# Kernel optimization log

Measured on AMD Instinct MI355X. Metric: run time of the kernel, lower is better.

Reference implementation:

```python
import jax, jax.numpy as jnp
import numpy as np

N = 100000
E = 1600000
NEG_SLOPE = 0.2


def _gat_layer(x, src, dst, W, a_src, a_dst, b, heads, out_ch):
    n = x.shape[0]
    h = (x @ W).reshape(n, heads, out_ch)                      # [N,H,C]
    alpha_src = (h * a_src).sum(-1)                            # [N,H]
    alpha_dst = (h * a_dst).sum(-1)                            # [N,H]
    e = jax.nn.leaky_relu(alpha_src[src] + alpha_dst[dst], NEG_SLOPE)  # [E,H]
    # segment softmax over incoming edges of each destination node
    m = jax.ops.segment_max(e, dst, num_segments=n)            # [N,H]
    ex = jnp.exp(e - m[dst])
    denom = jax.ops.segment_sum(ex, dst, num_segments=n)       # [N,H]
    alpha = ex / (denom[dst] + 1e-16)                          # [E,H]
    msg = h[src] * alpha[:, :, None]                           # [E,H,C]
    out = jax.ops.segment_sum(msg, dst, num_segments=n)        # [N,H,C]
    return out.reshape(n, heads * out_ch) + b


def setup_inputs() -> dict:
    key = jax.random.key(0)
    ks = jax.random.split(key, 10)
    glorot = lambda k, shape: jax.random.normal(k, shape, jnp.float32) * np.sqrt(2.0 / (shape[0] + shape[-1]))
    x = jax.random.normal(ks[0], (N, 5), jnp.float32)
    edge_index = jax.random.randint(ks[1], (2, E), 0, N, jnp.int64)
    return {
        "x": x,
        "edge_index": edge_index,
        "W1": glorot(ks[2], (5, 64)),
        "a_src1": glorot(ks[3], (8, 8)),
        "a_dst1": glorot(ks[4], (8, 8)),
        "b1": jnp.zeros((64,), jnp.float32),
        "W2": glorot(ks[5], (64, 2)),
        "a_src2": glorot(ks[6], (1, 2)),
        "a_dst2": glorot(ks[7], (1, 2)),
        "b2": jnp.zeros((2,), jnp.float32),
    }


def reference(x, edge_index, W1, a_src1, a_dst1, b1, W2, a_src2, a_dst2, b2):
    n = x.shape[0]
    loop = jnp.arange(n, dtype=edge_index.dtype)
    src = jnp.concatenate([edge_index[0], loop])   # PyG GATConv adds self-loops
    dst = jnp.concatenate([edge_index[1], loop])
    # dropout layers are no-ops in eval mode
    h = jax.nn.elu(_gat_layer(x, src, dst, W1, a_src1, a_dst1, b1, heads=8, out_ch=8))
    out = _gat_layer(h, src, dst, W2, a_src2, a_dst2, b2, heads=1, out_ch=2)
    return jax.nn.log_softmax(out, axis=1)
```

## Files before the change

### kernel.cpp

```cpp
#include <hip/hip_runtime.h>
#include <hip/hip_fp16.h>
#include <math.h>
#include <stdint.h>

#define N_NODES 100000
#define N_EDGES 1600000
#define NEG_SLOPE 0.2f
#define LOG2E 1.44269504088896340736f

#define CB     128
#define CBBITS 7
#define NCB    ((N_NODES + CB - 1) / CB)
#define TP     2048
#define NPB    ((N_EDGES + TP - 1) / TP)
#define WINB   2560
#define NB_NODE1 ((N_NODES * 8 + 511) / 512)
#define N8     ((size_t)N_NODES * 8)

typedef int nt_int4 __attribute__((ext_vector_type(4)));

__global__ void __launch_bounds__(512) k_np(
        const int* __restrict__ src, const int* __restrict__ dst,
        int* __restrict__ ofsT, unsigned* __restrict__ pairs,
        const float* __restrict__ x, const float* __restrict__ W1,
        const float* __restrict__ a_src1, const float* __restrict__ a_dst1,
        __half* __restrict__ xh, __half* __restrict__ as1h,
        float* __restrict__ ad1) {
    __shared__ int lcnt[1024];
    __shared__ unsigned stage[TP];
    __shared__ int wred[8];
    int t = threadIdx.x;

    if (blockIdx.x >= NPB) {
        int gid  = (blockIdx.x - NPB) * 512 + t;
        int n    = gid >> 3;
        int head = gid & 7;
        if (n >= N_NODES) return;

        float xv[5];
#pragma unroll
        for (int k = 0; k < 5; ++k) xv[k] = x[n * 5 + k];

        float as = 0.f, ad = 0.f;
#pragma unroll
        for (int j = 0; j < 8; ++j) {
            int c = head * 8 + j;
            float acc = 0.f;
#pragma unroll
            for (int k = 0; k < 5; ++k) acc += xv[k] * W1[k * 64 + c];
            as += acc * a_src1[c];
            ad += acc * a_dst1[c];
        }
        as1h[n * 8 + head] = __float2half(as * LOG2E);
        ad1[n * 8 + head] = ad * LOG2E;

        if (head == 0) {
            __half2 p0 = __halves2half2(__float2half(xv[0]), __float2half(xv[1]));
            __half2 p1 = __halves2half2(__float2half(xv[2]), __float2half(xv[3]));
            __half2 p2 = __halves2half2(__float2half(xv[4]), __float2half(0.f));
            __half2 p3 = __halves2half2(__float2half(0.f), __float2half(0.f));
            __half2* xp = (__half2*)&xh[(size_t)n * 8];
            xp[0] = p0; xp[1] = p1; xp[2] = p2; xp[3] = p3;
        }
        return;
    }

    int blk = blockIdx.x;
    int base = blk * TP + t * 4;
    bool act = base < N_EDGES;
    int nE = min(TP, N_EDGES - blk * TP);

    lcnt[t] = 0; lcnt[t + 512] = 0;
    __syncthreads();

    nt_int4 s4, d4;
    int myidx[4];
    if (act) {
        s4 = __builtin_nontemporal_load((const nt_int4*)(src + base));
        d4 = __builtin_nontemporal_load((const nt_int4*)(dst + base));
#pragma unroll
        for (int j = 0; j < 4; ++j)
            myidx[j] = atomicAdd(&lcnt[d4[j] >> CBBITS], 1);
    }
    __syncthreads();

    int b0 = lcnt[t * 2], b1 = lcnt[t * 2 + 1];
    int local = b0 + b1;
    int ln = t & 63, w = t >> 6;
    int sc = local;
#pragma unroll
    for (int off = 1; off < 64; off <<= 1) {
        int u = __shfl_up(sc, off, 64);
        if (ln >= off) sc += u;
    }
    if (ln == 63) wred[w] = sc;
    __syncthreads();
    if (t < 8) {
        int v = wred[t], s = v;
#pragma unroll
        for (int off = 1; off < 8; off <<= 1) {
            int u = __shfl_up(s, off, 8);
            if ((t & 7) >= off) s += u;
        }
        wred[t] = s - v;
    }
    __syncthreads();
    int run = wred[w] + sc - local;
    lcnt[t * 2] = run; lcnt[t * 2 + 1] = run + b0;
    if (t * 2     <= NCB) ofsT[(size_t)(t * 2)     * NPB + blk] = run;
    if (t * 2 + 1 <= NCB) ofsT[(size_t)(t * 2 + 1) * NPB + blk] = run + b0;
    __syncthreads();

    if (act) {
#pragma unroll
        for (int j = 0; j < 4; ++j) {
            int d = d4[j];
            stage[lcnt[d >> CBBITS] + myidx[j]] =
                ((unsigned)(d & (CB - 1)) << 17) | (unsigned)s4[j];
        }
    }
    __syncthreads();
    for (int i = t; i < nE; i += 512)
        pairs[(size_t)blk * TP + i] = stage[i];
}

__global__ void __launch_bounds__(512) k_csr(
        const int* __restrict__ ofsT, const unsigned* __restrict__ pairs,
        int* __restrict__ rbeg, int* __restrict__ rend, int* __restrict__ ssrc) {
    __shared__ unsigned stIn[WINB];
    __shared__ int stOut[WINB];
    __shared__ int o0s[NPB];
    __shared__ int cns[1026];
    __shared__ int lcnt[CB], lofs[CB], lcur[CB];
    __shared__ int wsum[2];
    __shared__ int wred[8];
    int B = blockIdx.x, t = threadIdx.x;
    int nvalid = min(CB, N_NODES - B * CB);
    int obase = B * WINB;

    for (int s = t; s < NPB; s += 512) {
        int o0 = ofsT[(size_t)B       * NPB + s];
        int o1 = ofsT[(size_t)(B + 1) * NPB + s];
        o0s[s] = o0;
        cns[s] = o1 - o0;
    }
    for (int s = NPB + t; s < 1024; s += 512) cns[s] = 0;
    if (t < CB) {
        lcnt[t] = (t < nvalid) ? 1 : 0;
        lcur[t] = 1;
    }
    __syncthreads();

    int a0 = cns[t * 2], a1 = cns[t * 2 + 1];
    int local = a0 + a1;
    int ln = t & 63, w = t >> 6;
    int sc2 = local;
#pragma unroll
    for (int off = 1; off < 64; off <<= 1) {
        int u = __shfl_up(sc2, off, 64);
        if (ln >= off) sc2 += u;
    }
    if (ln == 63) wred[w] = sc2;
    __syncthreads();
    if (t < 8) {
        int v = wred[t], s = v;
#pragma unroll
        for (int off = 1; off < 8; off <<= 1) {
            int u = __shfl_up(s, off, 8);
            if ((t & 7) >= off) s += u;
        }
        wred[t] = s - v;
    }
    __syncthreads();
    int run = wred[w] + sc2 - local;
    cns[t * 2] = run; cns[t * 2 + 1] = run + a0;
    __syncthreads();
    int m = cns[NPB];

    for (int i = t; i < m; i += 512) {
        int lo = 0, hi = NPB;
#pragma unroll
        for (int it = 0; it < 10; ++it) {
            int mid = (lo + hi + 1) >> 1;
            if (mid <= NPB && cns[mid] <= i) lo = mid; else hi = mid - 1;
        }
        int s = lo;
        unsigned r = pairs[(size_t)s * TP + o0s[s] + (i - cns[s])];
        stIn[i] = r;
        atomicAdd(&lcnt[r >> 17], 1);
    }
    __syncthreads();

    int v = (t < CB) ? lcnt[t] : 0;
    int wv = t >> 6;
    int sc = v;
#pragma unroll
    for (int off = 1; off < 64; off <<= 1) {
        int u = __shfl_up(sc, off, 64);
        if (ln >= off) sc += u;
    }
    if (ln == 63 && wv < 2) wsum[wv] = sc;
    __syncthreads();
    int wbase = (wv == 1) ? wsum[0] : 0;
    int ex = wbase + sc - v;
    if (t < CB) {
        lofs[t] = ex;
        int gi = B * CB + t;
        if (gi < N_NODES) {
            rbeg[gi] = obase + ex;
            rend[gi] = obase + ex + v;
            stOut[ex] = gi;
        }
    }
    __syncthreads();

    for (int k = t; k < m; k += 512) {
        unsigned p = stIn[k];
        int dl = p >> 17;
        int idx = atomicAdd(&lcur[dl], 1);
        stOut[lofs[dl] + idx] = (int)(p & 0x1FFFF);
    }
    __syncthreads();

    int tot = m + nvalid;
    for (int i = t; i < tot; i += 512) ssrc[obase + i] = stOut[i];
}

__global__ void __launch_bounds__(256) k_gather1(
        const int* __restrict__ rbeg, const int* __restrict__ rend,
        const int* __restrict__ ssrc, const float4* __restrict__ xh4,
        const __half* __restrict__ as1h, const float* __restrict__ ad1,
        float* __restrict__ xsbuf) {
    int gtid = blockIdx.x * blockDim.x + threadIdx.x;
    int d      = gtid >> 5;
    int lane32 = threadIdx.x & 31;
    if (d >= N_NODES) return;
    int e = lane32 >> 3;
    int h = lane32 & 7;

    int beg = rbeg[d], end = rend[d];
    float adv = ad1[d * 8 + h];
    float c0 = 0.f, c1 = 0.f, c2 = 0.f, c3 = 0.f, c4 = 0.f, den = 0.f;

    for (int k = beg; k < end; k += 8) {
        int kA = k + e, kB = k + 4 + e;
        bool vA = kA < end, vB = kB < end;
        int sA = ssrc[vA ? kA : beg];
        int sB = ssrc[vB ? kB : beg];
        float eA = __half2float(as1h[sA * 8 + h]);
        float eB = __half2float(as1h[sB * 8 + h]);
        float4 xA = xh4[sA];
        float4 xB = xh4[sB];
        float tA = eA + adv; tA = fmaxf(tA, NEG_SLOPE * tA);
        float tB = eB + adv; tB = fmaxf(tB, NEG_SLOPE * tB);
        float wA = vA ? __builtin_amdgcn_exp2f(tA) : 0.f;
        float wB = vB ? __builtin_amdgcn_exp2f(tB) : 0.f;
        float2 A01 = __half22float2(*(__half2*)&xA.x);
        float2 A23 = __half22float2(*(__half2*)&xA.y);
        float2 A4_ = __half22float2(*(__half2*)&xA.z);
        float2 B01 = __half22float2(*(__half2*)&xB.x);
        float2 B23 = __half22float2(*(__half2*)&xB.y);
        float2 B4_ = __half22float2(*(__half2*)&xB.z);
        c0 += wA * A01.x + wB * B01.x;
        c1 += wA * A01.y + wB * B01.y;
        c2 += wA * A23.x + wB * B23.x;
        c3 += wA * A23.y + wB * B23.y;
        c4 += wA * A4_.x + wB * B4_.x;
        den += wA + wB;
    }

#define REDH(x) x += __shfl_xor(x, 8, 64); x += __shfl_xor(x, 16, 64);
    REDH(c0) REDH(c1) REDH(c2) REDH(c3) REDH(c4) REDH(den)
#undef REDH

    if (e == 0) {
        float inv = 1.f / den;
        size_t idx = (size_t)d * 8 + h;
        xsbuf[idx]          = c0 * inv;
        xsbuf[N8 + idx]     = c1 * inv;
        xsbuf[2 * N8 + idx] = c2 * inv;
        xsbuf[3 * N8 + idx] = c3 * inv;
        xsbuf[4 * N8 + idx] = c4 * inv;
    }
}

__global__ void __launch_bounds__(256) k_rec(
        const float* __restrict__ xsbuf, const float* __restrict__ b1,
        const float* __restrict__ W1, const float* __restrict__ W2,
        const float* __restrict__ a_src2, const float* __restrict__ a_dst2,
        float4* __restrict__ rec) {
    int gtid = blockIdx.x * blockDim.x + threadIdx.x;
    int d = gtid >> 3;
    int h = gtid & 7;
    if (d >= N_NODES) return;

    size_t idx = (size_t)d * 8 + h;
    float xs[5] = { xsbuf[idx], xsbuf[N8 + idx], xsbuf[2 * N8 + idx],
                    xsbuf[3 * N8 + idx], xsbuf[4 * N8 + idx] };

    float4 hA = ((const float4*)b1)[2 * h];
    float4 hB = ((const float4*)b1)[2 * h + 1];
#pragma unroll
    for (int c = 0; c < 5; ++c) {
        float xc = xs[c];
        float4 wA = *(const float4*)(W1 + c * 64 + 8 * h);
        float4 wB = *(const float4*)(W1 + c * 64 + 8 * h + 4);
        hA.x += xc * wA.x; hA.y += xc * wA.y; hA.z += xc * wA.z; hA.w += xc * wA.w;
        hB.x += xc * wB.x; hB.y += xc * wB.y; hB.z += xc * wB.z; hB.w += xc * wB.w;
    }
    float v0 = hA.x, v1 = hA.y, v2 = hA.z, v3 = hA.w;
    float v4 = hB.x, v5 = hB.y, v6 = hB.z, v7 = hB.w;
    v0 = (v0 > 0.f) ? v0 : (__expf(v0) - 1.f);
    v1 = (v1 > 0.f) ? v1 : (__expf(v1) - 1.f);
    v2 = (v2 > 0.f) ? v2 : (__expf(v2) - 1.f);
    v3 = (v3 > 0.f) ? v3 : (__expf(v3) - 1.f);
    v4 = (v4 > 0.f) ? v4 : (__expf(v4) - 1.f);
    v5 = (v5 > 0.f) ? v5 : (__expf(v5) - 1.f);
    v6 = (v6 > 0.f) ? v6 : (__expf(v6) - 1.f);
    v7 = (v7 > 0.f) ? v7 : (__expf(v7) - 1.f);

    const float4* w4 = (const float4*)(W2 + h * 16);
    float4 wq0 = w4[0], wq1 = w4[1], wq2 = w4[2], wq3 = w4[3];
    float h20 = v0 * wq0.x + v1 * wq0.z + v2 * wq1.x + v3 * wq1.z
              + v4 * wq2.x + v5 * wq2.z + v6 * wq3.x + v7 * wq3.z;
    float h21 = v0 * wq0.y + v1 * wq0.w + v2 * wq1.y + v3 * wq1.w
              + v4 * wq2.y + v5 * wq2.w + v6 * wq3.y + v7 * wq3.w;
    h20 += __shfl_xor(h20, 1, 64); h20 += __shfl_xor(h20, 2, 64); h20 += __shfl_xor(h20, 4, 64);
    h21 += __shfl_xor(h21, 1, 64); h21 += __shfl_xor(h21, 2, 64); h21 += __shfl_xor(h21, 4, 64);

    if (h == 0) {
        float as2v = (h20 * a_src2[0] + h21 * a_src2[1]) * LOG2E;
        float ad2v = (h20 * a_dst2[0] + h21 * a_dst2[1]) * LOG2E;
        rec[d] = make_float4(h20, h21, as2v, ad2v);
    }
}

__global__ void __launch_bounds__(256) k_gather2(
        const int* __restrict__ rbeg, const int* __restrict__ rend,
        const int* __restrict__ ssrc, const float4* __restrict__ rec,
        const float* __restrict__ b2, float* __restrict__ out) {
    int gtid = blockIdx.x * blockDim.x + threadIdx.x;
    int d    = gtid >> 3;
    int lane = threadIdx.x & 7;
    if (d >= N_NODES) return;

    int beg = rbeg[d], end = rend[d];
    float adv = rec[d].w;
    float n0 = 0.f, n1 = 0.f, den = 0.f;
    for (int k = beg; k < end; k += 8) {
        int ki = k + lane;
        bool v = ki < end;
        int s = ssrc[v ? ki : beg];
        float4 r = rec[s];
        float t = r.z + adv; t = fmaxf(t, NEG_SLOPE * t);
        float w = v ? __builtin_amdgcn_exp2f(t) : 0.f;
        n0 += w * r.x; n1 += w * r.y; den += w;
    }
#pragma unroll
    for (int off = 1; off < 8; off <<= 1) {
        n0  += __shfl_xor(n0,  off, 8);
        n1  += __shfl_xor(n1,  off, 8);
        den += __shfl_xor(den, off, 8);
    }
    if (lane == 0) {
        float o0 = n0 / den + b2[0];
        float o1 = n1 / den + b2[1];
        float m  = fmaxf(o0, o1);
        float lse = m + __logf(__expf(o0 - m) + __expf(o1 - m));
        *(float2*)(out + (size_t)d * 2) = make_float2(o0 - lse, o1 - lse);
    }
}

extern "C" void kernel_launch(void* const* d_in, const int* in_sizes, int n_in,
                              void* d_out, int out_size, void* d_ws, size_t ws_size,
                              hipStream_t stream) {
    const float* x      = (const float*)d_in[0];
    const int*   ei     = (const int*)d_in[1];
    const float* W1     = (const float*)d_in[2];
    const float* a_src1 = (const float*)d_in[3];
    const float* a_dst1 = (const float*)d_in[4];
    const float* b1     = (const float*)d_in[5];
    const float* W2     = (const float*)d_in[6];
    const float* a_src2 = (const float*)d_in[7];
    const float* a_dst2 = (const float*)d_in[8];
    const float* b2     = (const float*)d_in[9];
    float* out = (float*)d_out;

    const int* src = ei;
    const int* dst = ei + N_EDGES;

    int* rbeg   = (int*)d_ws;
    int* rend   = rbeg + N_NODES;
    int* ssrc   = rend + N_NODES;
    uintptr_t pp = ((uintptr_t)(ssrc + (size_t)NCB * WINB) + 255) & ~(uintptr_t)255;
    float4*   rec  = (float4*)pp;
    float*    ad1  = (float*)(rec + N_NODES);
    __half*   as1h = (__half*)(ad1 + (size_t)N_NODES * 8);
    __half*   xh   = as1h + (size_t)N_NODES * 8;
    uintptr_t rg = ((uintptr_t)(xh + (size_t)N_NODES * 8) + 255) & ~(uintptr_t)255;
    int*      ofsT  = (int*)rg;
    unsigned* pairs = (unsigned*)(ofsT + (size_t)(NCB + 1) * NPB);
    float*    xsbuf = (float*)rg;

    k_np<<<NPB + NB_NODE1, 512, 0, stream>>>(src, dst, ofsT, pairs,
                                             x, W1, a_src1, a_dst1,
                                             xh, as1h, ad1);
    k_csr<<<NCB, 512, 0, stream>>>(ofsT, pairs, rbeg, rend, ssrc);
    k_gather1<<<(N_NODES * 32 + 255) / 256, 256, 0, stream>>>(rbeg, rend, ssrc,
                                                              (const float4*)xh,
                                                              as1h, ad1, xsbuf);
    k_rec<<<(N_NODES * 8 + 255) / 256, 256, 0, stream>>>(xsbuf, b1, W1, W2,
                                                         a_src2, a_dst2, rec);
    k_gather2<<<(N_NODES * 8 + 255) / 256, 256, 0, stream>>>(rbeg, rend, ssrc,
                                                             rec, b2, out);
}
```

Before: 156.6 us.

## Transpose offsets via tiled kernel, precompute slice IDs, halve gather1 lanes per node

k_np now writes its per-block bucket offsets row-major, so the writes are contiguous. A new shared-memory tiled transpose kernel then builds the column-major layout that k_csr reads. k_csr drops its per-element 10-step binary search and instead fills a slice-id lookup table in shared memory. k_gather1 uses 16 lanes per destination node instead of 32, which doubles the edges handled per lane and drops one reduction shuffle. The cost is one extra kernel launch, extra scratch memory, and more serial per-thread work on high-degree nodes.

```diff
diff --git a/kernel.cpp b/kernel.cpp
--- a/kernel.cpp
+++ b/kernel.cpp
@@ -16,12 +16,13 @@
 #define WINB   2560
 #define NB_NODE1 ((N_NODES * 8 + 511) / 512)
 #define N8     ((size_t)N_NODES * 8)
+#define NTT    25
 
 typedef int nt_int4 __attribute__((ext_vector_type(4)));
 
 __global__ void __launch_bounds__(512) k_np(
         const int* __restrict__ src, const int* __restrict__ dst,
-        int* __restrict__ ofsT, unsigned* __restrict__ pairs,
+        int* __restrict__ ofs, unsigned* __restrict__ pairs,
         const float* __restrict__ x, const float* __restrict__ W1,
         const float* __restrict__ a_src1, const float* __restrict__ a_dst1,
         __half* __restrict__ xh, __half* __restrict__ as1h,
@@ -107,8 +108,9 @@
     __syncthreads();
     int run = wred[w] + sc - local;
     lcnt[t * 2] = run; lcnt[t * 2 + 1] = run + b0;
-    if (t * 2     <= NCB) ofsT[(size_t)(t * 2)     * NPB + blk] = run;
-    if (t * 2 + 1 <= NCB) ofsT[(size_t)(t * 2 + 1) * NPB + blk] = run + b0;
+    int* orow = ofs + (size_t)blk * (NCB + 1);
+    if (t * 2     <= NCB) orow[t * 2]     = run;
+    if (t * 2 + 1 <= NCB) orow[t * 2 + 1] = run + b0;
     __syncthreads();
 
     if (act) {
@@ -122,6 +124,29 @@
     __syncthreads();
     for (int i = t; i < nE; i += 512)
         pairs[(size_t)blk * TP + i] = stage[i];
+}
+
+__global__ void __launch_bounds__(256) k_tr(
+        const int* __restrict__ ofs, int* __restrict__ ofsT) {
+    __shared__ int tile[32][33];
+    int bx = blockIdx.x % NTT;
+    int by = blockIdx.x / NTT;
+    int tx = threadIdx.x & 31, ty = threadIdx.x >> 5;
+#pragma unroll
+    for (int i = 0; i < 4; ++i) {
+        int r = by * 32 + ty + 8 * i;
+        int c = bx * 32 + tx;
+        tile[ty + 8 * i][tx] = (r < NPB && c <= NCB)
+                             ? ofs[(size_t)r * (NCB + 1) + c] : 0;
+    }
+    __syncthreads();
+#pragma unroll
+    for (int i = 0; i < 4; ++i) {
+        int c = bx * 32 + ty + 8 * i;
+        int r = by * 32 + tx;
+        if (c <= NCB && r < NPB)
+            ofsT[(size_t)c * NPB + r] = tile[tx][ty + 8 * i];
+    }
 }
 
 __global__ void __launch_bounds__(512) k_csr(
@@ -129,6 +154,7 @@
         int* __restrict__ rbeg, int* __restrict__ rend, int* __restrict__ ssrc) {
     __shared__ unsigned stIn[WINB];
     __shared__ int stOut[WINB];
+    __shared__ unsigned short sliceId[WINB];
     __shared__ int o0s[NPB];
     __shared__ int cns[1026];
     __shared__ int lcnt[CB], lofs[CB], lcur[CB];
@@ -177,14 +203,14 @@
     __syncthreads();
     int m = cns[NPB];
 
+    for (int s = t; s < NPB; s += 512) {
+        int j0 = cns[s], j1 = cns[s + 1];
+        for (int j = j0; j < j1; ++j) sliceId[j] = (unsigned short)s;
+    }
+    __syncthreads();
+
     for (int i = t; i < m; i += 512) {
-        int lo = 0, hi = NPB;
-#pragma unroll
-        for (int it = 0; it < 10; ++it) {
-            int mid = (lo + hi + 1) >> 1;
-            if (mid <= NPB && cns[mid] <= i) lo = mid; else hi = mid - 1;
-        }
-        int s = lo;
+        int s = sliceId[i];
         unsigned r = pairs[(size_t)s * TP + o0s[s] + (i - cns[s])];
         stIn[i] = r;
         atomicAdd(&lcnt[r >> 17], 1);
@@ -232,18 +258,18 @@
         const __half* __restrict__ as1h, const float* __restrict__ ad1,
         float* __restrict__ xsbuf) {
     int gtid = blockIdx.x * blockDim.x + threadIdx.x;
-    int d      = gtid >> 5;
-    int lane32 = threadIdx.x & 31;
+    int d      = gtid >> 4;
+    int lane16 = threadIdx.x & 15;
     if (d >= N_NODES) return;
-    int e = lane32 >> 3;
-    int h = lane32 & 7;
+    int e = lane16 >> 3;
+    int h = lane16 & 7;
 
     int beg = rbeg[d], end = rend[d];
     float adv = ad1[d * 8 + h];
     float c0 = 0.f, c1 = 0.f, c2 = 0.f, c3 = 0.f, c4 = 0.f, den = 0.f;
 
-    for (int k = beg; k < end; k += 8) {
-        int kA = k + e, kB = k + 4 + e;
+    for (int k = beg; k < end; k += 4) {
+        int kA = k + e, kB = k + 2 + e;
         bool vA = kA < end, vB = kB < end;
         int sA = ssrc[vA ? kA : beg];
         int sB = ssrc[vB ? kB : beg];
@@ -269,7 +295,7 @@
         den += wA + wB;
     }
 
-#define REDH(x) x += __shfl_xor(x, 8, 64); x += __shfl_xor(x, 16, 64);
+#define REDH(x) x += __shfl_xor(x, 8, 64);
     REDH(c0) REDH(c1) REDH(c2) REDH(c3) REDH(c4) REDH(den)
 #undef REDH
 
@@ -398,15 +424,17 @@
     __half*   as1h = (__half*)(ad1 + (size_t)N_NODES * 8);
     __half*   xh   = as1h + (size_t)N_NODES * 8;
     uintptr_t rg = ((uintptr_t)(xh + (size_t)N_NODES * 8) + 255) & ~(uintptr_t)255;
-    int*      ofsT  = (int*)rg;
+    int*      ofs   = (int*)rg;
+    int*      ofsT  = ofs + (size_t)NPB * (NCB + 1);
     unsigned* pairs = (unsigned*)(ofsT + (size_t)(NCB + 1) * NPB);
     float*    xsbuf = (float*)rg;
 
-    k_np<<<NPB + NB_NODE1, 512, 0, stream>>>(src, dst, ofsT, pairs,
+    k_np<<<NPB + NB_NODE1, 512, 0, stream>>>(src, dst, ofs, pairs,
                                              x, W1, a_src1, a_dst1,
                                              xh, as1h, ad1);
+    k_tr<<<NTT * NTT, 256, 0, stream>>>(ofs, ofsT);
     k_csr<<<NCB, 512, 0, stream>>>(ofsT, pairs, rbeg, rend, ssrc);
-    k_gather1<<<(N_NODES * 32 + 255) / 256, 256, 0, stream>>>(rbeg, rend, ssrc,
+    k_gather1<<<(N_NODES * 16 + 255) / 256, 256, 0, stream>>>(rbeg, rend, ssrc,
                                                               (const float4*)xh,
                                                               as1h, ad1, xsbuf);
     k_rec<<<(N_NODES * 8 + 255) / 256, 256, 0, stream>>>(xsbuf, b1, W1, W2,
```

New measurement: 156.1 us. No clear change (-0.3%).
